# Optimization experiments

Measured on AMD Instinct MI355X. Metric: run time of the kernel, lower is better.

The kernel has to match this reference:

```python
import jax, jax.numpy as jnp
import numpy as np
import math

B, T, D, SLOTS, TOPK = 8, 4096, 512, 128, 8


def setup_inputs() -> dict:
    key = jax.random.key(0)
    kq, kK, kV = jax.random.split(key, 3)
    # xavier_uniform for [slots, d_model]: bound = sqrt(6/(slots+d_model))
    bound = math.sqrt(6.0 / (SLOTS + D))
    return {
        "q": jax.random.normal(kq, (B, T, D), dtype=jnp.float32),
        "K": jax.random.uniform(kK, (SLOTS, D), minval=-bound, maxval=bound, dtype=jnp.float32),
        "V": jax.random.uniform(kV, (SLOTS, D), minval=-bound, maxval=bound, dtype=jnp.float32),
        "salience": jnp.zeros((SLOTS,), dtype=jnp.float32),
        "topk": TOPK,
    }


def reference(q, K, V, salience, topk):
    # q: [B,T,D], K/V: [S,D], salience: [S]
    Bq, Tq, Dq = q.shape
    k = min(topk, K.shape[0])
    scores = jnp.einsum('btd,sd->bts', q, K) / jnp.sqrt(jnp.float32(Dq))
    scores = scores + salience[None, None, :]
    topk_scores, topk_indices = jax.lax.top_k(scores, k)          # [B,T,k]
    attention_weights = jax.nn.softmax(topk_scores, axis=-1)      # [B,T,k]
    V_selected = V[topk_indices]                                  # [B,T,k,D] gather
    read_vectors = jnp.einsum('btk,btkd->btd', attention_weights, V_selected)
    return read_vectors, attention_weights
```

## Files before the change

### kernel.cpp

```cpp
#include <hip/hip_runtime.h>
#include <hip/hip_bf16.h>
#include <math.h>

#define R_TOTAL 32768
#define DM      512
#define NSLOT   128
#define KSEL    8

typedef _Float16 half8 __attribute__((ext_vector_type(8)));
typedef float    floatx4 __attribute__((ext_vector_type(4)));

__global__ void smb_splitK(const float* __restrict__ Km,
                           _Float16* __restrict__ K1, _Float16* __restrict__ K2) {
  const int i = blockIdx.x * 256 + threadIdx.x;
  const float f = Km[i] * 256.0f;
  const _Float16 h = (_Float16)f;
  K1[i] = h;
  K2[i] = (_Float16)(f - (float)h);
}

__device__ __forceinline__ void load16_lds(const _Float16* g, _Float16* l) {
  __builtin_amdgcn_global_load_lds(
      (const __attribute__((address_space(1))) unsigned int*)g,
      (__attribute__((address_space(3))) unsigned int*)l, 16, 0, 0);
}

__global__ __launch_bounds__(256, 2) void smb_main(
    const float* __restrict__ q,
    const _Float16* __restrict__ K1,
    const _Float16* __restrict__ K2,
    const float* __restrict__ Vm,
    const float* __restrict__ sal,
    float* __restrict__ outv,
    float* __restrict__ outw)
{
  __shared__ _Float16 stage[2][8][NSLOT][8];
  __shared__ float slab[4][16][132];

  const int t  = threadIdx.x;
  const int w  = t >> 6;
  const int l  = t & 63;
  const int li = l & 15;
  const int kg = l >> 4;
  const int r0w = blockIdx.x * 64 + w * 16;

  const float* qrow = q + (size_t)(r0w + li) * DM + kg * 8;

  const int u0 = 2 * w;

  floatx4 acc[8];
#pragma unroll
  for (int g = 0; g < 8; ++g) acc[g] = (floatx4){0.f, 0.f, 0.f, 0.f};

#pragma unroll
  for (int i = 0; i < 4; ++i) {
    const int u = u0 + (i >> 1);
    const int p = i & 1;
    const _Float16* src = (u < 4 ? K1 : K2) + (size_t)(p * 64 + l) * DM + (u & 3) * 8;
    load16_lds(src, &stage[0][u][p * 64][0]);
  }
  float4 q0c = *(const float4*)(qrow + 0);
  float4 q1c = *(const float4*)(qrow + 4);
  __syncthreads();

#pragma unroll 2
  for (int c = 0; c < 16; ++c) {
    const int cb = c & 1, nb = cb ^ 1;
    float4 q0n, q1n;
    if (c < 15) {
#pragma unroll
      for (int i = 0; i < 4; ++i) {
        const int u = u0 + (i >> 1);
        const int p = i & 1;
        const _Float16* src = (u < 4 ? K1 : K2)
                            + (size_t)(p * 64 + l) * DM + (c + 1) * 32 + (u & 3) * 8;
        load16_lds(src, &stage[nb][u][p * 64][0]);
      }
      q0n = *(const float4*)(qrow + (c + 1) * 32);
      q1n = *(const float4*)(qrow + (c + 1) * 32 + 4);
    }

    half8 a1, a2;
#pragma unroll
    for (int j = 0; j < 4; ++j) {
      const float f0 = q0c[j] * 16.0f;
      const float f1 = q1c[j] * 16.0f;
      const _Float16 h0 = (_Float16)f0;
      const _Float16 h1 = (_Float16)f1;
      a1[j]     = h0;  a2[j]     = (_Float16)(f0 - (float)h0);
      a1[4 + j] = h1;  a2[4 + j] = (_Float16)(f1 - (float)h1);
    }
#pragma unroll
    for (int g = 0; g < 8; ++g) {
      const half8 b1 = *(const half8*)&stage[cb][kg][g * 16 + li][0];
      const half8 b2 = *(const half8*)&stage[cb][4 + kg][g * 16 + li][0];
      acc[g] = __builtin_amdgcn_mfma_f32_16x16x32_f16(a1, b1, acc[g], 0, 0, 0);
      acc[g] = __builtin_amdgcn_mfma_f32_16x16x32_f16(a2, b1, acc[g], 0, 0, 0);
      acc[g] = __builtin_amdgcn_mfma_f32_16x16x32_f16(a1, b2, acc[g], 0, 0, 0);
    }
    q0c = q0n; q1c = q1n;
    __syncthreads();
  }

  const float den = sqrtf((float)DM);
#pragma unroll
  for (int g = 0; g < 8; ++g) {
    const float sv = sal[g * 16 + li];
#pragma unroll
    for (int i = 0; i < 4; ++i) {
      const float s = (acc[g][i] * 0.000244140625f) / den + sv;
      slab[w][kg * 4 + i][g * 16 + li] = s;
    }
  }
  asm volatile("s_waitcnt lgkmcnt(0)" ::: "memory");

  const int row = l >> 2;
  const int lq  = l & 3;

  float bs[8]; int bi[8];
#pragma unroll
  for (int p = 0; p < 8; ++p) { bs[p] = -3.0e38f; bi[p] = 0x7fffffff; }

#pragma unroll
  for (int jj = 0; jj < 32; ++jj) {
    const int   j = jj * 4 + lq;
    const float s = slab[w][row][j];
    bool c[8];
#pragma unroll
    for (int p = 0; p < 8; ++p) c[p] = s > bs[p];
    float nb[8]; int ni[8];
    nb[0] = c[0] ? s : bs[0];
    ni[0] = c[0] ? j : bi[0];
#pragma unroll
    for (int p = 7; p >= 1; --p) {
      nb[p] = c[p] ? (c[p - 1] ? bs[p - 1] : s) : bs[p];
      ni[p] = c[p] ? (c[p - 1] ? bi[p - 1] : j) : bi[p];
    }
#pragma unroll
    for (int p = 0; p < 8; ++p) { bs[p] = nb[p]; bi[p] = ni[p]; }
  }

  float ts[8]; int ti_[8];
#pragma unroll
  for (int r = 0; r < 8; ++r) {
    float hs = bs[0]; int hi = bi[0];
    {
      const float os = __shfl_xor(hs, 1, 64);
      const int   oi = __shfl_xor(hi, 1, 64);
      if (os > hs || (os == hs && oi < hi)) { hs = os; hi = oi; }
    }
    {
      const float os = __shfl_xor(hs, 2, 64);
      const int   oi = __shfl_xor(hi, 2, 64);
      if (os > hs || (os == hs && oi < hi)) { hs = os; hi = oi; }
    }
    ts[r] = hs; ti_[r] = hi;
    if (bs[0] == hs && bi[0] == hi) {
#pragma unroll
      for (int p = 0; p < 7; ++p) { bs[p] = bs[p + 1]; bi[p] = bi[p + 1]; }
      bs[7] = -3.0e38f; bi[7] = 0x7fffffff;
    }
  }

  float tw[8];
  const float mx = ts[0];
  float esum = 0.0f;
#pragma unroll
  for (int r = 0; r < 8; ++r) { tw[r] = expf(ts[r] - mx); esum += tw[r]; }
#pragma unroll
  for (int r = 0; r < 8; ++r) tw[r] /= esum;

  if (lq == 0) {
#pragma unroll
    for (int r = 0; r < 8; ++r) outw[(size_t)(r0w + row) * KSEL + r] = tw[r];
  }

  const float4* __restrict__ V4 = (const float4*)Vm;
  float4* __restrict__ O4 = (float4*)outv;
  const size_t obase = (size_t)(r0w + row) * (DM / 4);
#pragma unroll 4
  for (int cc = 0; cc < 32; ++cc) {
    const int cdx = cc * 4 + lq;
    float4 a; a.x = a.y = a.z = a.w = 0.0f;
#pragma unroll
    for (int r = 0; r < 8; ++r) {
      const float4 v = V4[(size_t)ti_[r] * (DM / 4) + cdx];
      a.x = fmaf(tw[r], v.x, a.x);
      a.y = fmaf(tw[r], v.y, a.y);
      a.z = fmaf(tw[r], v.z, a.z);
      a.w = fmaf(tw[r], v.w, a.w);
    }
    O4[obase + cdx] = a;
  }
}

extern "C" void kernel_launch(void* const* d_in, const int* in_sizes, int n_in,
                              void* d_out, int out_size, void* d_ws, size_t ws_size,
                              hipStream_t stream) {
  const float* q   = (const float*)d_in[0];
  const float* Km  = (const float*)d_in[1];
  const float* Vm  = (const float*)d_in[2];
  const float* sal = (const float*)d_in[3];

  float* outv = (float*)d_out;
  float* outw = outv + (size_t)R_TOTAL * DM;

  _Float16* K1 = (_Float16*)d_ws;
  _Float16* K2 = K1 + (size_t)NSLOT * DM;

  hipLaunchKernelGGL(smb_splitK, dim3((NSLOT * DM) / 256), dim3(256), 0, stream, Km, K1, K2);
  hipLaunchKernelGGL(smb_main, dim3(R_TOTAL / 64), dim3(256), 0, stream,
                     q, K1, K2, Vm, sal, outv, outw);
}
```

Measured before the change: 68.96 us.

## Double threads per block by splitting slot columns across wave pairs

Moves to 512-thread blocks in which each pair of waves shares a 16-row group and splits the 128 slots into two halves. Each wave now holds 4 MFMA accumulators instead of 8 and issues half the K staging loads. The top-k and the V gather use 8 lanes per row instead of 4. The aim is more waves in flight and less per-wave work to hide latency, at the cost of a block-wide barrier before top-k and one extra shuffle level in the merge.

```diff
diff --git a/kernel.cpp b/kernel.cpp
--- a/kernel.cpp
+++ b/kernel.cpp
@@ -25,7 +25,7 @@
       (__attribute__((address_space(3))) unsigned int*)l, 16, 0, 0);
 }
 
-__global__ __launch_bounds__(256, 2) void smb_main(
+__global__ __launch_bounds__(512, 4) void smb_main(
     const float* __restrict__ q,
     const _Float16* __restrict__ K1,
     const _Float16* __restrict__ K2,
@@ -35,29 +35,28 @@
     float* __restrict__ outw)
 {
   __shared__ _Float16 stage[2][8][NSLOT][8];
-  __shared__ float slab[4][16][132];
+  __shared__ float slab[64][132];
 
   const int t  = threadIdx.x;
   const int w  = t >> 6;
   const int l  = t & 63;
   const int li = l & 15;
   const int kg = l >> 4;
-  const int r0w = blockIdx.x * 64 + w * 16;
+  const int rg = w >> 1;
+  const int sh = w & 1;
+  const int r0b = blockIdx.x * 64;
+  const int r0w = r0b + rg * 16;
 
   const float* qrow = q + (size_t)(r0w + li) * DM + kg * 8;
 
-  const int u0 = 2 * w;
-
-  floatx4 acc[8];
-#pragma unroll
-  for (int g = 0; g < 8; ++g) acc[g] = (floatx4){0.f, 0.f, 0.f, 0.f};
-
-#pragma unroll
-  for (int i = 0; i < 4; ++i) {
-    const int u = u0 + (i >> 1);
-    const int p = i & 1;
-    const _Float16* src = (u < 4 ? K1 : K2) + (size_t)(p * 64 + l) * DM + (u & 3) * 8;
-    load16_lds(src, &stage[0][u][p * 64][0]);
+  floatx4 acc[4];
+#pragma unroll
+  for (int g = 0; g < 4; ++g) acc[g] = (floatx4){0.f, 0.f, 0.f, 0.f};
+
+#pragma unroll
+  for (int p = 0; p < 2; ++p) {
+    const _Float16* src = (w < 4 ? K1 : K2) + (size_t)(p * 64 + l) * DM + (w & 3) * 8;
+    load16_lds(src, &stage[0][w][p * 64][0]);
   }
   float4 q0c = *(const float4*)(qrow + 0);
   float4 q1c = *(const float4*)(qrow + 4);
@@ -69,12 +68,10 @@
     float4 q0n, q1n;
     if (c < 15) {
 #pragma unroll
-      for (int i = 0; i < 4; ++i) {
-        const int u = u0 + (i >> 1);
-        const int p = i & 1;
-        const _Float16* src = (u < 4 ? K1 : K2)
-                            + (size_t)(p * 64 + l) * DM + (c + 1) * 32 + (u & 3) * 8;
-        load16_lds(src, &stage[nb][u][p * 64][0]);
+      for (int p = 0; p < 2; ++p) {
+        const _Float16* src = (w < 4 ? K1 : K2)
+                            + (size_t)(p * 64 + l) * DM + (c + 1) * 32 + (w & 3) * 8;
+        load16_lds(src, &stage[nb][w][p * 64][0]);
       }
       q0n = *(const float4*)(qrow + (c + 1) * 32);
       q1n = *(const float4*)(qrow + (c + 1) * 32 + 4);
@@ -91,9 +88,10 @@
       a1[4 + j] = h1;  a2[4 + j] = (_Float16)(f1 - (float)h1);
     }
 #pragma unroll
-    for (int g = 0; g < 8; ++g) {
-      const half8 b1 = *(const half8*)&stage[cb][kg][g * 16 + li][0];
-      const half8 b2 = *(const half8*)&stage[cb][4 + kg][g * 16 + li][0];
+    for (int g = 0; g < 4; ++g) {
+      const int slot = sh * 64 + g * 16 + li;
+      const half8 b1 = *(const half8*)&stage[cb][kg][slot][0];
+      const half8 b2 = *(const half8*)&stage[cb][4 + kg][slot][0];
       acc[g] = __builtin_amdgcn_mfma_f32_16x16x32_f16(a1, b1, acc[g], 0, 0, 0);
       acc[g] = __builtin_amdgcn_mfma_f32_16x16x32_f16(a2, b1, acc[g], 0, 0, 0);
       acc[g] = __builtin_amdgcn_mfma_f32_16x16x32_f16(a1, b2, acc[g], 0, 0, 0);
@@ -104,27 +102,28 @@
 
   const float den = sqrtf((float)DM);
 #pragma unroll
-  for (int g = 0; g < 8; ++g) {
-    const float sv = sal[g * 16 + li];
+  for (int g = 0; g < 4; ++g) {
+    const int col = sh * 64 + g * 16 + li;
+    const float sv = sal[col];
 #pragma unroll
     for (int i = 0; i < 4; ++i) {
       const float s = (acc[g][i] * 0.000244140625f) / den + sv;
-      slab[w][kg * 4 + i][g * 16 + li] = s;
-    }
-  }
-  asm volatile("s_waitcnt lgkmcnt(0)" ::: "memory");
-
-  const int row = l >> 2;
-  const int lq  = l & 3;
+      slab[rg * 16 + kg * 4 + i][col] = s;
+    }
+  }
+  __syncthreads();
+
+  const int row = t >> 3;
+  const int lq  = t & 7;
 
   float bs[8]; int bi[8];
 #pragma unroll
   for (int p = 0; p < 8; ++p) { bs[p] = -3.0e38f; bi[p] = 0x7fffffff; }
 
 #pragma unroll
-  for (int jj = 0; jj < 32; ++jj) {
-    const int   j = jj * 4 + lq;
-    const float s = slab[w][row][j];
+  for (int jj = 0; jj < 16; ++jj) {
+    const int   j = jj * 8 + lq;
+    const float s = slab[row][j];
     bool c[8];
 #pragma unroll
     for (int p = 0; p < 8; ++p) c[p] = s > bs[p];
@@ -144,14 +143,10 @@
 #pragma unroll
   for (int r = 0; r < 8; ++r) {
     float hs = bs[0]; int hi = bi[0];
-    {
-      const float os = __shfl_xor(hs, 1, 64);
-      const int   oi = __shfl_xor(hi, 1, 64);
-      if (os > hs || (os == hs && oi < hi)) { hs = os; hi = oi; }
-    }
-    {
-      const float os = __shfl_xor(hs, 2, 64);
-      const int   oi = __shfl_xor(hi, 2, 64);
+#pragma unroll
+    for (int m = 1; m <= 4; m <<= 1) {
+      const float os = __shfl_xor(hs, m, 64);
+      const int   oi = __shfl_xor(hi, m, 64);
       if (os > hs || (os == hs && oi < hi)) { hs = os; hi = oi; }
     }
     ts[r] = hs; ti_[r] = hi;
@@ -172,15 +167,15 @@
 
   if (lq == 0) {
 #pragma unroll
-    for (int r = 0; r < 8; ++r) outw[(size_t)(r0w + row) * KSEL + r] = tw[r];
+    for (int r = 0; r < 8; ++r) outw[(size_t)(r0b + row) * KSEL + r] = tw[r];
   }
 
   const float4* __restrict__ V4 = (const float4*)Vm;
   float4* __restrict__ O4 = (float4*)outv;
-  const size_t obase = (size_t)(r0w + row) * (DM / 4);
+  const size_t obase = (size_t)(r0b + row) * (DM / 4);
 #pragma unroll 4
-  for (int cc = 0; cc < 32; ++cc) {
-    const int cdx = cc * 4 + lq;
+  for (int cc = 0; cc < 16; ++cc) {
+    const int cdx = cc * 8 + lq;
     float4 a; a.x = a.y = a.z = a.w = 0.0f;
 #pragma unroll
     for (int r = 0; r < 8; ++r) {
@@ -209,6 +204,6 @@
   _Float16* K2 = K1 + (size_t)NSLOT * DM;
 
   hipLaunchKernelGGL(smb_splitK, dim3((NSLOT * DM) / 256), dim3(256), 0, stream, Km, K1, K2);
-  hipLaunchKernelGGL(smb_main, dim3(R_TOTAL / 64), dim3(256), 0, stream,
+  hipLaunchKernelGGL(smb_main, dim3(R_TOTAL / 64), dim3(512), 0, stream,
                      q, K1, K2, Vm, sal, outv, outw);
 }
```

Result: no change. 67.67 us (-1.9%).
